# Kernel tuning notes

Hardware: AMD Instinct MI355X
Metric: run time of the kernel (lower is better)

## Reference

```python
import math
import jax, jax.numpy as jnp
import numpy as np

N_GRAPHS = 400
N_PER = 50
N = N_GRAPHS * N_PER          # 20000 nodes
K = 12                        # k_neighbors
E = N * K                     # 240000 edges
ND = 128                      # node_dim
TD = 128                      # time_dim
LD = 128                      # latent_dim
SD = 32                       # species_emb_dim
L = 4                         # num_layers


def _lin(key, fi, fo):
    return (jax.random.normal(key, (fi, fo), dtype=jnp.float32) / np.sqrt(fi)).astype(jnp.float32)


def setup_inputs() -> dict:
    rng = np.random.default_rng(0)
    coords = (rng.standard_normal((N_GRAPHS, N_PER, 3)) * 3.0).astype(np.float32)
    # exact kNN per graph (loop=False): dst = center node, src = neighbor
    d = ((coords[:, :, None, :] - coords[:, None, :, :]) ** 2).sum(-1)  # [G, n, n]
    ii = np.arange(N_PER)
    d[:, ii, ii] = np.inf
    nbr = np.argpartition(d, K, axis=-1)[:, :, :K]                      # [G, n, K]
    base = (np.arange(N_GRAPHS) * N_PER)[:, None, None]
    edge_src = (nbr + base).reshape(-1).astype(np.int64)
    edge_dst = (np.broadcast_to(ii[None, :, None], (N_GRAPHS, N_PER, K)) + base).reshape(-1).astype(np.int64)
    batch_indices = np.repeat(np.arange(N_GRAPHS), N_PER).astype(np.int64)

    key = jax.random.key(0)
    ks = jax.random.split(key, 32)
    inp = {
        'z_nodes': jax.random.normal(ks[0], (N, LD), dtype=jnp.float32),
        't': jax.random.uniform(ks[1], (N_GRAPHS,), dtype=jnp.float32) * 1000.0,
        'cart_coords': jnp.asarray(coords.reshape(N, 3)),
        'species': jax.random.randint(ks[2], (N,), 1, 119),
        'batch_indices': jnp.asarray(batch_indices),
        'edge_src': jnp.asarray(edge_src),
        'edge_dst': jnp.asarray(edge_dst),
        # parameters
        'species_emb': jax.random.normal(ks[3], (119, SD), dtype=jnp.float32),
        'tm_W1': _lin(ks[4], TD, 2 * TD), 'tm_b1': jnp.zeros((2 * TD,), jnp.float32),
        'tm_W2': _lin(ks[5], 2 * TD, TD), 'tm_b2': jnp.zeros((TD,), jnp.float32),
        'ne_W': _lin(ks[6], LD + SD, ND), 'ne_b': jnp.zeros((ND,), jnp.float32),
        'eW1': jnp.stack([_lin(jax.random.fold_in(ks[7], l), 2 * ND + 1 + TD, ND) for l in range(L)]),
        'eb1': jnp.zeros((L, ND), jnp.float32),
        'eW2': jnp.stack([_lin(jax.random.fold_in(ks[8], l), ND, ND) for l in range(L)]),
        'eb2': jnp.zeros((L, ND), jnp.float32),
        'cW1': jnp.stack([_lin(jax.random.fold_in(ks[9], l), ND, ND) for l in range(L)]),
        'cb1': jnp.zeros((L, ND), jnp.float32),
        'cW2': jnp.stack([_lin(jax.random.fold_in(ks[10], l), ND, 1) for l in range(L)]),
        'nW1': jnp.stack([_lin(jax.random.fold_in(ks[11], l), 2 * ND + TD, ND) for l in range(L)]),
        'nb1': jnp.zeros((L, ND), jnp.float32),
        'nW2': jnp.stack([_lin(jax.random.fold_in(ks[12], l), ND, ND) for l in range(L)]),
        'nb2': jnp.zeros((L, ND), jnp.float32),
    }
    return inp


def reference(z_nodes, t, cart_coords, species, batch_indices, edge_src, edge_dst,
              species_emb, tm_W1, tm_b1, tm_W2, tm_b2, ne_W, ne_b,
              eW1, eb1, eW2, eb2, cW1, cb1, cW2, nW1, nb1, nW2, nb2):
    silu = jax.nn.silu
    # sinusoidal time embedding + time MLP
    half = TD // 2
    freqs = jnp.exp(jnp.arange(half, dtype=jnp.float32) * (-math.log(10000.0) / (half - 1)))
    ang = t[:, None] * freqs[None, :]                     # [G, half]
    temb = jnp.concatenate([jnp.sin(ang), jnp.cos(ang)], axis=-1)
    temb = silu(temb @ tm_W1 + tm_b1) @ tm_W2 + tm_b2     # [G, TD]
    t_nodes = temb[batch_indices]                         # [N, TD]

    sp = species_emb[species]                             # [N, SD]
    h = jnp.concatenate([z_nodes, sp], axis=-1) @ ne_W + ne_b  # [N, ND]

    diff = cart_coords[edge_src] - cart_coords[edge_dst]  # [E, 3]
    dist_sq = jnp.sum(diff * diff, axis=-1, keepdims=True)  # [E, 1]
    dist = jnp.sqrt(dist_sq + 1e-8)
    t_edges = t_nodes[edge_src]                           # [E, TD]

    n = h.shape[0]
    total_shift = jnp.zeros_like(cart_coords)
    for l in range(L):
        edge_in = jnp.concatenate([h[edge_src], h[edge_dst], dist_sq, t_edges], axis=-1)
        m = silu(edge_in @ eW1[l] + eb1[l])
        m = silu(m @ eW2[l] + eb2[l])                     # [E, ND]
        gate = silu(m @ cW1[l] + cb1[l]) @ cW2[l]         # [E, 1]
        shift = diff / dist * gate                        # [E, 3]
        total_shift = total_shift + jax.ops.segment_sum(shift, edge_dst, num_segments=n)
        m_i = jax.ops.segment_sum(m, edge_dst, num_segments=n)  # [N, ND]
        node_in = jnp.concatenate([h, m_i, t_nodes], axis=-1)
        h = h + (silu(node_in @ nW1[l] + nb1[l]) @ nW2[l] + nb2[l])
    return (total_shift, h)
```

## Files before the change

kernel.cpp:

```cpp
#include <hip/hip_runtime.h>
#include <math.h>

#define GN 400
#define NPER 50
#define NN 20000
#define LL 4

typedef __attribute__((ext_vector_type(8))) short short8;
typedef __attribute__((ext_vector_type(4))) float f32x4;

__device__ __forceinline__ float fast_rcp(float x) {
#if __has_builtin(__builtin_amdgcn_rcpf)
  return __builtin_amdgcn_rcpf(x);
#else
  return 1.0f / x;
#endif
}
__device__ __forceinline__ float silu_f(float x) {
  return x * fast_rcp(1.0f + __expf(-x));
}
__device__ __forceinline__ unsigned short f2bu(float f) {
  unsigned int u = __float_as_uint(f);
  unsigned int r = (u + 0x7fffu + ((u >> 16) & 1u)) >> 16;
  return (unsigned short)r;
}
__device__ __forceinline__ unsigned int pack2bf(float lo, float hi) {
  unsigned int a = __float_as_uint(lo) + 0x8000u;
  unsigned int b = __float_as_uint(hi) + 0x8000u;
#if __has_builtin(__builtin_amdgcn_perm)
  return __builtin_amdgcn_perm(b, a, 0x07060302);
#else
  return (b & 0xffff0000u) | (a >> 16);
#endif
}
__device__ __forceinline__ float bhi(unsigned int u) { return __uint_as_float(u & 0xffff0000u); }
__device__ __forceinline__ float blo(unsigned int u) { return __uint_as_float(u << 16); }

__device__ __forceinline__ short8 pack8(const float* v) {
  union { unsigned int u[4]; short8 s; } t;
  t.u[0] = pack2bf(v[0], v[1]);
  t.u[1] = pack2bf(v[2], v[3]);
  t.u[2] = pack2bf(v[4], v[5]);
  t.u[3] = pack2bf(v[6], v[7]);
  return t.s;
}

__global__ __launch_bounds__(128) void time_kernel(
    const float* __restrict__ t,
    const float* __restrict__ tm_W1, const float* __restrict__ tm_b1,
    const float* __restrict__ tm_W2, const float* __restrict__ tm_b2,
    const float* __restrict__ eW1, const float* __restrict__ eb1,
    const float* __restrict__ nW1, const float* __restrict__ nb1,
    float* __restrict__ temb, float* __restrict__ tE, float* __restrict__ tN)
{
  int g = blockIdx.x;
  int j = threadIdx.x;
  __shared__ float x[128];
  __shared__ float hid[256];
  __shared__ float te[128];
  float tv = t[g];
  if (j < 64) {
    float f = __expf((float)j * (-9.210340371976184f / 63.0f));
    float a = tv * f;
    x[j] = sinf(a);
    x[j + 64] = cosf(a);
  }
  __syncthreads();
  for (int o = j; o < 256; o += 128) {
    float acc = tm_b1[o];
    for (int k = 0; k < 128; ++k) acc = fmaf(x[k], tm_W1[k * 256 + o], acc);
    hid[o] = silu_f(acc);
  }
  __syncthreads();
  {
    float acc = tm_b2[j];
    for (int k = 0; k < 256; ++k) acc = fmaf(hid[k], tm_W2[k * 128 + j], acc);
    te[j] = acc;
    temb[g * 128 + j] = acc;
  }
  __syncthreads();
  for (int l = 0; l < LL; ++l) {
    const float* W = eW1 + (l * 385 + 257) * 128;
    float acc = eb1[l * 128 + j];
    for (int k = 0; k < 128; ++k) acc = fmaf(te[k], W[k * 128 + j], acc);
    tE[(l * GN + g) * 128 + j] = acc;
    const float* Wn = nW1 + (l * 384 + 256) * 128;
    float acc2 = nb1[l * 128 + j];
    for (int k = 0; k < 128; ++k) acc2 = fmaf(te[k], Wn[k * 128 + j], acc2);
    tN[(l * GN + g) * 128 + j] = acc2;
  }
}

__global__ __launch_bounds__(256) void prep_transpose(
    const float* __restrict__ eW1, const float* __restrict__ eW2,
    const float* __restrict__ cW1, const float* __restrict__ nW1,
    const float* __restrict__ nW2, const float* __restrict__ ne_W,
    unsigned short* __restrict__ eABt, unsigned short* __restrict__ eW2t,
    unsigned short* __restrict__ cW1t, unsigned short* __restrict__ nW1t,
    unsigned short* __restrict__ nW2t, unsigned short* __restrict__ ne_Wt)
{
  __shared__ float tile[32][33];
  int j = blockIdx.y;
  const float* src;
  unsigned short* dst;
  int dstride = 128, Kj = 128;
  if (j < 28) {
    int l = j / 7, m = j % 7;
    switch (m) {
      case 0: src = eW1 + (l * 385 + 0) * 128;   dst = eABt + l * 256 * 128;             break;
      case 1: src = eW1 + (l * 385 + 128) * 128; dst = eABt + l * 256 * 128 + 128 * 128; break;
      case 2: src = eW2 + l * 16384;             dst = eW2t + l * 16384;                 break;
      case 3: src = cW1 + l * 16384;             dst = cW1t + l * 16384;                 break;
      case 4: src = nW1 + (l * 384 + 0) * 128;   dst = nW1t + l * 128 * 256; dstride = 256; break;
      case 5: src = nW1 + (l * 384 + 128) * 128; dst = nW1t + l * 128 * 256 + 128; dstride = 256; break;
      default: src = nW2 + l * 16384;            dst = nW2t + l * 16384;                 break;
    }
  } else {
    src = ne_W; dst = ne_Wt; dstride = 160; Kj = 160;
  }
  int gx = blockIdx.x;
  int tk = (gx % 5) * 32;
  int tn = (gx / 5) * 32;
  if (tk >= Kj) return;
  int ti = threadIdx.x >> 5, tj = threadIdx.x & 31;
#pragma unroll
  for (int p = 0; p < 4; ++p) {
    int i = ti + p * 8;
    tile[i][tj] = src[(tk + i) * 128 + tn + tj];
  }
  __syncthreads();
#pragma unroll
  for (int p = 0; p < 4; ++p) {
    int i = ti + p * 8;
    dst[(tn + i) * dstride + tk + tj] = f2bu(tile[tj][i]);
  }
}

__global__ __launch_bounds__(128) void edge_mfma(
    const unsigned short* __restrict__ hAB,
    const float* __restrict__ coords, const int* __restrict__ edge_src,
    const float* __restrict__ eW1,
    const unsigned short* __restrict__ eW2t, const float* __restrict__ eb2,
    const unsigned short* __restrict__ cW1t, const float* __restrict__ cb1,
    const float* __restrict__ cW2, const float* __restrict__ tE,
    unsigned short* __restrict__ m_i, float* __restrict__ shift_out,
    int l, int addflag)
{
  __shared__ unsigned short mbuf[2][48 * 136];
  __shared__ float sdir[2][48 * 4];
  __shared__ float sgate[2][48];

  int tid = threadIdx.x;
  int wv = tid >> 6;
  int l6 = tid & 63;
  int e16 = l6 & 15, q = l6 >> 4;
  int nbase = blockIdx.x * 8 + wv * 4;
  int ebase = nbase * 12;
  unsigned short* mb = mbuf[wv];
  float* sd = sdir[wv];
  float* sg = sgate[wv];

  const unsigned short* eW2t_l = eW2t + l * 16384;
  const unsigned short* cW1t_l = cW1t + l * 16384;
  const float* eb2_l = eb2 + l * 128;
  const float* cb1_l = cb1 + l * 128;
  const float* cW2_l = cW2 + l * 128;
  const float* tE_l = tE + l * GN * 128;
  const float* wd = eW1 + (l * 385 + 256) * 128;

  int ssrc[3], sdst[3];
  float sds[3];
#pragma unroll
  for (int grp = 0; grp < 3; ++grp) {
    int eloc = grp * 16 + e16;
    int e = ebase + eloc;
    int src = edge_src[e];
    src = min(max(src, 0), NN - 1);
    int dst = nbase + eloc / 12;
    float dx = coords[src * 3 + 0] - coords[dst * 3 + 0];
    float dy = coords[src * 3 + 1] - coords[dst * 3 + 1];
    float dz = coords[src * 3 + 2] - coords[dst * 3 + 2];
    float ds = dx * dx + dy * dy + dz * dz;
    float rinv = 1.0f / sqrtf(ds + 1e-8f);
    if (q == 0) {
      sd[eloc * 4 + 0] = dx * rinv;
      sd[eloc * 4 + 1] = dy * rinv;
      sd[eloc * 4 + 2] = dz * rinv;
    }
    ssrc[grp] = src; sdst[grp] = dst; sds[grp] = ds;
  }

  short8 bfr[3][4];
#pragma unroll
  for (int grp = 0; grp < 3; ++grp) {
    int g = sdst[grp] / NPER;
    float ds = sds[grp];
#pragma unroll
    for (int kc = 0; kc < 4; ++kc) {
      int k0 = kc * 32 + q * 8;
      uint4 ua = *(const uint4*)(hAB + ssrc[grp] * 256 + k0);
      uint4 ub = *(const uint4*)(hAB + sdst[grp] * 256 + 128 + k0);
      float4 w0 = *(const float4*)(wd + k0);
      float4 w1 = *(const float4*)(wd + k0 + 4);
      float4 t0 = *(const float4*)(tE_l + g * 128 + k0);
      float4 t1 = *(const float4*)(tE_l + g * 128 + k0 + 4);
      float v[8];
      v[0] = silu_f(blo(ua.x) + blo(ub.x) + ds * w0.x + t0.x);
      v[1] = silu_f(bhi(ua.x) + bhi(ub.x) + ds * w0.y + t0.y);
      v[2] = silu_f(blo(ua.y) + blo(ub.y) + ds * w0.z + t0.z);
      v[3] = silu_f(bhi(ua.y) + bhi(ub.y) + ds * w0.w + t0.w);
      v[4] = silu_f(blo(ua.z) + blo(ub.z) + ds * w1.x + t1.x);
      v[5] = silu_f(bhi(ua.z) + bhi(ub.z) + ds * w1.y + t1.y);
      v[6] = silu_f(blo(ua.w) + blo(ub.w) + ds * w1.z + t1.z);
      v[7] = silu_f(bhi(ua.w) + bhi(ub.w) + ds * w1.w + t1.w);
      bfr[grp][kc] = pack8(v);
    }
  }

#pragma unroll
  for (int mt = 0; mt < 8; ++mt) {
    short8 af[4];
#pragma unroll
    for (int kc = 0; kc < 4; ++kc)
      af[kc] = *(const short8*)(eW2t_l + (mt * 16 + e16) * 128 + kc * 32 + q * 8);
    f32x4 acc[3] = {(f32x4){0,0,0,0}, (f32x4){0,0,0,0}, (f32x4){0,0,0,0}};
#pragma unroll
    for (int kc = 0; kc < 4; ++kc) {
#pragma unroll
      for (int grp = 0; grp < 3; ++grp)
        acc[grp] = __builtin_amdgcn_mfma_f32_16x16x32_bf16(af[kc], bfr[grp][kc], acc[grp], 0, 0, 0);
    }
    float4 b4 = *(const float4*)(eb2_l + mt * 16 + q * 4);
#pragma unroll
    for (int grp = 0; grp < 3; ++grp) {
      float v0 = silu_f(acc[grp][0] + b4.x);
      float v1 = silu_f(acc[grp][1] + b4.y);
      float v2 = silu_f(acc[grp][2] + b4.z);
      float v3 = silu_f(acc[grp][3] + b4.w);
      uint2 p;
      p.x = pack2bf(v0, v1);
      p.y = pack2bf(v2, v3);
      *(uint2*)&mb[(grp * 16 + e16) * 136 + mt * 16 + q * 4] = p;
    }
  }
  __threadfence_block();

  short8 af2[3][4];
#pragma unroll
  for (int grp = 0; grp < 3; ++grp)
#pragma unroll
    for (int kc = 0; kc < 4; ++kc)
      af2[grp][kc] = *(const short8*)&mb[(grp * 16 + e16) * 136 + kc * 32 + q * 8];

  float gp[3][4] = {{0,0,0,0},{0,0,0,0},{0,0,0,0}};
#pragma unroll
  for (int ct = 0; ct < 8; ++ct) {
    short8 bf[4];
#pragma unroll
    for (int kc = 0; kc < 4; ++kc)
      bf[kc] = *(const short8*)(cW1t_l + (ct * 16 + e16) * 128 + kc * 32 + q * 8);
    f32x4 acc[3] = {(f32x4){0,0,0,0}, (f32x4){0,0,0,0}, (f32x4){0,0,0,0}};
#pragma unroll
    for (int kc = 0; kc < 4; ++kc) {
#pragma unroll
      for (int grp = 0; grp < 3; ++grp)
        acc[grp] = __builtin_amdgcn_mfma_f32_16x16x32_bf16(af2[grp][kc], bf[kc], acc[grp], 0, 0, 0);
    }
    float cb = cb1_l[ct * 16 + e16];
    float c2 = cW2_l[ct * 16 + e16];
#pragma unroll
    for (int grp = 0; grp < 3; ++grp)
#pragma unroll
      for (int r = 0; r < 4; ++r)
        gp[grp][r] += silu_f(acc[grp][r] + cb) * c2;
  }
#pragma unroll
  for (int grp = 0; grp < 3; ++grp)
#pragma unroll
    for (int r = 0; r < 4; ++r) {
      float v = gp[grp][r];
      v += __shfl_xor(v, 1);
      v += __shfl_xor(v, 2);
      v += __shfl_xor(v, 4);
      v += __shfl_xor(v, 8);
      if (e16 == 0) sg[grp * 16 + q * 4 + r] = v;
    }
  __threadfence_block();

  {
    int nl = q, c8 = e16 * 8;
    float s[8] = {0,0,0,0,0,0,0,0};
#pragma unroll
    for (int r = 0; r < 12; ++r) {
      uint4 u = *(const uint4*)&mb[(nl * 12 + r) * 136 + c8];
      s[0] += blo(u.x); s[1] += bhi(u.x);
      s[2] += blo(u.y); s[3] += bhi(u.y);
      s[4] += blo(u.z); s[5] += bhi(u.z);
      s[6] += blo(u.w); s[7] += bhi(u.w);
    }
    uint4 o;
    o.x = pack2bf(s[0], s[1]); o.y = pack2bf(s[2], s[3]);
    o.z = pack2bf(s[4], s[5]); o.w = pack2bf(s[6], s[7]);
    *(uint4*)(m_i + (nbase + nl) * 128 + c8) = o;
  }
  if (l6 < 12) {
    int nl = l6 / 3, c = l6 - nl * 3;
    float s = 0.f;
#pragma unroll
    for (int r = 0; r < 12; ++r) {
      int e = nl * 12 + r;
      s = fmaf(sd[e * 4 + c], sg[e], s);
    }
    int n = nbase + nl;
    if (addflag) shift_out[n * 3 + c] += s;
    else         shift_out[n * 3 + c] = s;
  }
}

__global__ __launch_bounds__(128) void node_mfma(
    float* __restrict__ h, const unsigned short* __restrict__ m_i,
    const unsigned short* __restrict__ nW1t_l, const unsigned short* __restrict__ nW2t_l,
    const float* __restrict__ nb2_l, const float* __restrict__ tN_l,
    const unsigned short* __restrict__ eABt_next, unsigned short* __restrict__ hAB,
    int has_c)
{
  __shared__ unsigned short z1buf[16 * 136];
  __shared__ unsigned short hbuf[16 * 136];
  int tid = threadIdx.x;
  int wv = tid >> 6, l6 = tid & 63;
  int e16 = l6 & 15, q = l6 >> 4;
  int row = blockIdx.x * 16 + e16;
  int g = row / NPER;

  short8 bfh[8];
#pragma unroll
  for (int kc = 0; kc < 8; ++kc) {
    int k0 = kc * 32 + q * 8;
    if (k0 < 128) {
      float4 f0 = *(const float4*)(h + row * 128 + k0);
      float4 f1 = *(const float4*)(h + row * 128 + k0 + 4);
      float v[8] = {f0.x, f0.y, f0.z, f0.w, f1.x, f1.y, f1.z, f1.w};
      bfh[kc] = pack8(v);
    } else {
      bfh[kc] = *(const short8*)(m_i + row * 128 + (k0 - 128));
    }
  }
#pragma unroll
  for (int mi = 0; mi < 4; ++mi) {
    int mt = wv * 4 + mi;
    short8 af[8];
#pragma unroll
    for (int kc = 0; kc < 8; ++kc)
      af[kc] = *(const short8*)(nW1t_l + (mt * 16 + e16) * 256 + kc * 32 + q * 8);
    f32x4 acc = (f32x4){0,0,0,0};
#pragma unroll
    for (int kc = 0; kc < 8; ++kc)
      acc = __builtin_amdgcn_mfma_f32_16x16x32_bf16(af[kc], bfh[kc], acc, 0, 0, 0);
    float4 tv = *(const float4*)(tN_l + g * 128 + mt * 16 + q * 4);
    float v0 = silu_f(acc[0] + tv.x);
    float v1 = silu_f(acc[1] + tv.y);
    float v2 = silu_f(acc[2] + tv.z);
    float v3 = silu_f(acc[3] + tv.w);
    uint2 p; p.x = pack2bf(v0, v1); p.y = pack2bf(v2, v3);
    *(uint2*)&z1buf[e16 * 136 + mt * 16 + q * 4] = p;
  }
  __syncthreads();

  short8 zf[4];
#pragma unroll
  for (int kc = 0; kc < 4; ++kc)
    zf[kc] = *(const short8*)&z1buf[e16 * 136 + kc * 32 + q * 8];
#pragma unroll
  for (int mi = 0; mi < 4; ++mi) {
    int mt = wv * 4 + mi;
    short8 af[4];
#pragma unroll
    for (int kc = 0; kc < 4; ++kc)
      af[kc] = *(const short8*)(nW2t_l + (mt * 16 + e16) * 128 + kc * 32 + q * 8);
    f32x4 acc = (f32x4){0,0,0,0};
#pragma unroll
    for (int kc = 0; kc < 4; ++kc)
      acc = __builtin_amdgcn_mfma_f32_16x16x32_bf16(af[kc], zf[kc], acc, 0, 0, 0);
    float4 hv = *(const float4*)(h + row * 128 + mt * 16 + q * 4);
    float4 b4 = *(const float4*)(nb2_l + mt * 16 + q * 4);
    float4 o;
    o.x = hv.x + acc[0] + b4.x;
    o.y = hv.y + acc[1] + b4.y;
    o.z = hv.z + acc[2] + b4.z;
    o.w = hv.w + acc[3] + b4.w;
    *(float4*)(h + row * 128 + mt * 16 + q * 4) = o;
    uint2 p; p.x = pack2bf(o.x, o.y); p.y = pack2bf(o.z, o.w);
    *(uint2*)&hbuf[e16 * 136 + mt * 16 + q * 4] = p;
  }
  if (has_c) {
    __syncthreads();
    short8 hf[4];
#pragma unroll
    for (int kc = 0; kc < 4; ++kc)
      hf[kc] = *(const short8*)&hbuf[e16 * 136 + kc * 32 + q * 8];
#pragma unroll
    for (int mi = 0; mi < 8; ++mi) {
      int mt = wv * 8 + mi;
      short8 af[4];
#pragma unroll
      for (int kc = 0; kc < 4; ++kc)
        af[kc] = *(const short8*)(eABt_next + (mt * 16 + e16) * 128 + kc * 32 + q * 8);
      f32x4 acc = (f32x4){0,0,0,0};
#pragma unroll
      for (int kc = 0; kc < 4; ++kc)
        acc = __builtin_amdgcn_mfma_f32_16x16x32_bf16(af[kc], hf[kc], acc, 0, 0, 0);
      uint2 p; p.x = pack2bf(acc[0], acc[1]); p.y = pack2bf(acc[2], acc[3]);
      *(uint2*)(hAB + row * 256 + mt * 16 + q * 4) = p;
    }
  }
}

__global__ __launch_bounds__(128) void encoder_mfma(
    const float* __restrict__ z, const int* __restrict__ species,
    const float* __restrict__ species_emb,
    const unsigned short* __restrict__ ne_Wt, const float* __restrict__ ne_b,
    const unsigned short* __restrict__ eABt0,
    float* __restrict__ h, unsigned short* __restrict__ hAB)
{
  __shared__ unsigned short hbuf[16 * 136];
  int tid = threadIdx.x;
  int wv = tid >> 6, l6 = tid & 63;
  int e16 = l6 & 15, q = l6 >> 4;
  int row = blockIdx.x * 16 + e16;
  int sp = species[row];
  sp = min(max(sp, 0), 118);

  short8 bfh[5];
#pragma unroll
  for (int kc = 0; kc < 5; ++kc) {
    int k0 = kc * 32 + q * 8;
    const float* src = (k0 < 128) ? (z + row * 128 + k0)
                                  : (species_emb + sp * 32 + (k0 - 128));
    float4 f0 = *(const float4*)src;
    float4 f1 = *(const float4*)(src + 4);
    float v[8] = {f0.x, f0.y, f0.z, f0.w, f1.x, f1.y, f1.z, f1.w};
    bfh[kc] = pack8(v);
  }
#pragma unroll
  for (int mi = 0; mi < 4; ++mi) {
    int mt = wv * 4 + mi;
    short8 af[5];
#pragma unroll
    for (int kc = 0; kc < 5; ++kc)
      af[kc] = *(const short8*)(ne_Wt + (mt * 16 + e16) * 160 + kc * 32 + q * 8);
    f32x4 acc = (f32x4){0,0,0,0};
#pragma unroll
    for (int kc = 0; kc < 5; ++kc)
      acc = __builtin_amdgcn_mfma_f32_16x16x32_bf16(af[kc], bfh[kc], acc, 0, 0, 0);
    float4 b4 = *(const float4*)(ne_b + mt * 16 + q * 4);
    float4 o;
    o.x = acc[0] + b4.x; o.y = acc[1] + b4.y;
    o.z = acc[2] + b4.z; o.w = acc[3] + b4.w;
    *(float4*)(h + row * 128 + mt * 16 + q * 4) = o;
    uint2 p; p.x = pack2bf(o.x, o.y); p.y = pack2bf(o.z, o.w);
    *(uint2*)&hbuf[e16 * 136 + mt * 16 + q * 4] = p;
  }
  __syncthreads();
  short8 hf[4];
#pragma unroll
  for (int kc = 0; kc < 4; ++kc)
    hf[kc] = *(const short8*)&hbuf[e16 * 136 + kc * 32 + q * 8];
#pragma unroll
  for (int mi = 0; mi < 8; ++mi) {
    int mt = wv * 8 + mi;
    short8 af[4];
#pragma unroll
    for (int kc = 0; kc < 4; ++kc)
      af[kc] = *(const short8*)(eABt0 + (mt * 16 + e16) * 128 + kc * 32 + q * 8);
    f32x4 acc = (f32x4){0,0,0,0};
#pragma unroll
    for (int kc = 0; kc < 4; ++kc)
      acc = __builtin_amdgcn_mfma_f32_16x16x32_bf16(af[kc], hf[kc], acc, 0, 0, 0);
    uint2 p; p.x = pack2bf(acc[0], acc[1]); p.y = pack2bf(acc[2], acc[3]);
    *(uint2*)(hAB + row * 256 + mt * 16 + q * 4) = p;
  }
}

extern "C" void kernel_launch(void* const* d_in, const int* in_sizes, int n_in,
                              void* d_out, int out_size, void* d_ws, size_t ws_size,
                              hipStream_t stream)
{
  const float* z_nodes     = (const float*)d_in[0];
  const float* t           = (const float*)d_in[1];
  const float* coords      = (const float*)d_in[2];
  const int*   species     = (const int*)d_in[3];
  const int*   edge_src    = (const int*)d_in[5];
  const float* species_emb = (const float*)d_in[7];
  const float* tm_W1 = (const float*)d_in[8];
  const float* tm_b1 = (const float*)d_in[9];
  const float* tm_W2 = (const float*)d_in[10];
  const float* tm_b2 = (const float*)d_in[11];
  const float* ne_W  = (const float*)d_in[12];
  const float* ne_b  = (const float*)d_in[13];
  const float* eW1   = (const float*)d_in[14];
  const float* eb1   = (const float*)d_in[15];
  const float* eW2   = (const float*)d_in[16];
  const float* eb2   = (const float*)d_in[17];
  const float* cW1   = (const float*)d_in[18];
  const float* cb1   = (const float*)d_in[19];
  const float* cW2   = (const float*)d_in[20];
  const float* nW1   = (const float*)d_in[21];
  const float* nb1   = (const float*)d_in[22];
  const float* nW2   = (const float*)d_in[23];
  const float* nb2   = (const float*)d_in[24];

  char* wsb = (char*)d_ws;
  float* temb = (float*)(wsb + 0);
  float* tEb  = (float*)(wsb + 204800);
  float* tNb  = (float*)(wsb + 1024000);
  unsigned short* hAB  = (unsigned short*)(wsb + 1843200);
  unsigned short* m_i  = (unsigned short*)(wsb + 12083200);
  unsigned short* eABt = (unsigned short*)(wsb + 17203200);
  unsigned short* eW2t = (unsigned short*)(wsb + 17465344);
  unsigned short* cW1t = (unsigned short*)(wsb + 17596416);
  unsigned short* nW1t = (unsigned short*)(wsb + 17727488);
  unsigned short* nW2t = (unsigned short*)(wsb + 17989632);
  unsigned short* ne_Wt= (unsigned short*)(wsb + 18120704);

  float* outp  = (float*)d_out;
  float* shift = outp;
  float* h     = outp + 60000;

  time_kernel<<<GN, 128, 0, stream>>>(t, tm_W1, tm_b1, tm_W2, tm_b2,
                                      eW1, eb1, nW1, nb1, temb, tEb, tNb);
  prep_transpose<<<dim3(20, 29), 256, 0, stream>>>(eW1, eW2, cW1, nW1, nW2, ne_W,
                                                   eABt, eW2t, cW1t, nW1t, nW2t, ne_Wt);
  encoder_mfma<<<NN / 16, 128, 0, stream>>>(z_nodes, species, species_emb,
                                            ne_Wt, ne_b, eABt, h, hAB);
  for (int l = 0; l < LL; ++l) {
    edge_mfma<<<NN / 8, 128, 0, stream>>>(hAB, coords, edge_src, eW1,
                                          eW2t, eb2, cW1t, cb1, cW2, tEb,
                                          m_i, shift, l, (l > 0) ? 1 : 0);
    int has_c = (l < LL - 1) ? 1 : 0;
    node_mfma<<<NN / 16, 128, 0, stream>>>(h, m_i,
                                           nW1t + l * 128 * 256, nW2t + l * 16384,
                                           nb2 + l * 128, tNb + l * GN * 128,
                                           has_c ? (eABt + (l + 1) * 256 * 128) : eABt,
                                           hAB, has_c);
  }
}
```

Baseline: 554.8 us.

## Give each wave its own 16-row tile in node/encoder kernels, drop block barriers

```diff
diff --git a/kernel.cpp b/kernel.cpp
--- a/kernel.cpp
+++ b/kernel.cpp
@@ -43,6 +43,13 @@
   t.u[2] = pack2bf(v[4], v[5]);
   t.u[3] = pack2bf(v[6], v[7]);
   return t.s;
+}
+__device__ __forceinline__ void wave_fence() {
+#if __has_builtin(__builtin_amdgcn_wave_barrier)
+  __builtin_amdgcn_wave_barrier();
+#else
+  __syncthreads();
+#endif
 }
 
 __global__ __launch_bounds__(128) void time_kernel(
@@ -243,7 +250,7 @@
       *(uint2*)&mb[(grp * 16 + e16) * 136 + mt * 16 + q * 4] = p;
     }
   }
-  __threadfence_block();
+  wave_fence();
 
   short8 af2[3][4];
 #pragma unroll
@@ -285,7 +292,7 @@
       v += __shfl_xor(v, 8);
       if (e16 == 0) sg[grp * 16 + q * 4 + r] = v;
     }
-  __threadfence_block();
+  wave_fence();
 
   {
     int nl = q, c8 = e16 * 8;
@@ -324,13 +331,15 @@
     const unsigned short* __restrict__ eABt_next, unsigned short* __restrict__ hAB,
     int has_c)
 {
-  __shared__ unsigned short z1buf[16 * 136];
-  __shared__ unsigned short hbuf[16 * 136];
+  __shared__ unsigned short z1buf[2][16 * 136];
+  __shared__ unsigned short hbuf[2][16 * 136];
   int tid = threadIdx.x;
   int wv = tid >> 6, l6 = tid & 63;
   int e16 = l6 & 15, q = l6 >> 4;
-  int row = blockIdx.x * 16 + e16;
+  int row = blockIdx.x * 32 + wv * 16 + e16;
   int g = row / NPER;
+  unsigned short* zb = z1buf[wv];
+  unsigned short* hb = hbuf[wv];
 
   short8 bfh[8];
 #pragma unroll
@@ -346,8 +355,7 @@
     }
   }
 #pragma unroll
-  for (int mi = 0; mi < 4; ++mi) {
-    int mt = wv * 4 + mi;
+  for (int mt = 0; mt < 8; ++mt) {
     short8 af[8];
 #pragma unroll
     for (int kc = 0; kc < 8; ++kc)
@@ -362,17 +370,16 @@
     float v2 = silu_f(acc[2] + tv.z);
     float v3 = silu_f(acc[3] + tv.w);
     uint2 p; p.x = pack2bf(v0, v1); p.y = pack2bf(v2, v3);
-    *(uint2*)&z1buf[e16 * 136 + mt * 16 + q * 4] = p;
-  }
-  __syncthreads();
+    *(uint2*)&zb[e16 * 136 + mt * 16 + q * 4] = p;
+  }
+  wave_fence();
 
   short8 zf[4];
 #pragma unroll
   for (int kc = 0; kc < 4; ++kc)
-    zf[kc] = *(const short8*)&z1buf[e16 * 136 + kc * 32 + q * 8];
-#pragma unroll
-  for (int mi = 0; mi < 4; ++mi) {
-    int mt = wv * 4 + mi;
+    zf[kc] = *(const short8*)&zb[e16 * 136 + kc * 32 + q * 8];
+#pragma unroll
+  for (int mt = 0; mt < 8; ++mt) {
     short8 af[4];
 #pragma unroll
     for (int kc = 0; kc < 4; ++kc)
@@ -390,17 +397,16 @@
     o.w = hv.w + acc[3] + b4.w;
     *(float4*)(h + row * 128 + mt * 16 + q * 4) = o;
     uint2 p; p.x = pack2bf(o.x, o.y); p.y = pack2bf(o.z, o.w);
-    *(uint2*)&hbuf[e16 * 136 + mt * 16 + q * 4] = p;
+    *(uint2*)&hb[e16 * 136 + mt * 16 + q * 4] = p;
   }
   if (has_c) {
-    __syncthreads();
+    wave_fence();
     short8 hf[4];
 #pragma unroll
     for (int kc = 0; kc < 4; ++kc)
-      hf[kc] = *(const short8*)&hbuf[e16 * 136 + kc * 32 + q * 8];
-#pragma unroll
-    for (int mi = 0; mi < 8; ++mi) {
-      int mt = wv * 8 + mi;
+      hf[kc] = *(const short8*)&hb[e16 * 136 + kc * 32 + q * 8];
+#pragma unroll
+    for (int mt = 0; mt < 16; ++mt) {
       short8 af[4];
 #pragma unroll
       for (int kc = 0; kc < 4; ++kc)
@@ -422,11 +428,12 @@
     const unsigned short* __restrict__ eABt0,
     float* __restrict__ h, unsigned short* __restrict__ hAB)
 {
-  __shared__ unsigned short hbuf[16 * 136];
+  __shared__ unsigned short hbuf[2][16 * 136];
   int tid = threadIdx.x;
   int wv = tid >> 6, l6 = tid & 63;
   int e16 = l6 & 15, q = l6 >> 4;
-  int row = blockIdx.x * 16 + e16;
+  int row = blockIdx.x * 32 + wv * 16 + e16;
+  unsigned short* hb = hbuf[wv];
   int sp = species[row];
   sp = min(max(sp, 0), 118);
 
@@ -442,8 +449,7 @@
     bfh[kc] = pack8(v);
   }
 #pragma unroll
-  for (int mi = 0; mi < 4; ++mi) {
-    int mt = wv * 4 + mi;
+  for (int mt = 0; mt < 8; ++mt) {
     short8 af[5];
 #pragma unroll
     for (int kc = 0; kc < 5; ++kc)
@@ -458,16 +464,15 @@
     o.z = acc[2] + b4.z; o.w = acc[3] + b4.w;
     *(float4*)(h + row * 128 + mt * 16 + q * 4) = o;
     uint2 p; p.x = pack2bf(o.x, o.y); p.y = pack2bf(o.z, o.w);
-    *(uint2*)&hbuf[e16 * 136 + mt * 16 + q * 4] = p;
-  }
-  __syncthreads();
+    *(uint2*)&hb[e16 * 136 + mt * 16 + q * 4] = p;
+  }
+  wave_fence();
   short8 hf[4];
 #pragma unroll
   for (int kc = 0; kc < 4; ++kc)
-    hf[kc] = *(const short8*)&hbuf[e16 * 136 + kc * 32 + q * 8];
-#pragma unroll
-  for (int mi = 0; mi < 8; ++mi) {
-    int mt = wv * 8 + mi;
+    hf[kc] = *(const short8*)&hb[e16 * 136 + kc * 32 + q * 8];
+#pragma unroll
+  for (int mt = 0; mt < 16; ++mt) {
     short8 af[4];
 #pragma unroll
     for (int kc = 0; kc < 4; ++kc)
@@ -530,14 +535,14 @@
                                       eW1, eb1, nW1, nb1, temb, tEb, tNb);
   prep_transpose<<<dim3(20, 29), 256, 0, stream>>>(eW1, eW2, cW1, nW1, nW2, ne_W,
                                                    eABt, eW2t, cW1t, nW1t, nW2t, ne_Wt);
-  encoder_mfma<<<NN / 16, 128, 0, stream>>>(z_nodes, species, species_emb,
+  encoder_mfma<<<NN / 32, 128, 0, stream>>>(z_nodes, species, species_emb,
                                             ne_Wt, ne_b, eABt, h, hAB);
   for (int l = 0; l < LL; ++l) {
     edge_mfma<<<NN / 8, 128, 0, stream>>>(hAB, coords, edge_src, eW1,
                                           eW2t, eb2, cW1t, cb1, cW2, tEb,
                                           m_i, shift, l, (l > 0) ? 1 : 0);
     int has_c = (l < LL - 1) ? 1 : 0;
-    node_mfma<<<NN / 16, 128, 0, stream>>>(h, m_i,
+    node_mfma<<<NN / 32, 128, 0, stream>>>(h, m_i,
                                            nW1t + l * 128 * 256, nW2t + l * 16384,
                                            nb2 + l * 128, tNb + l * GN * 128,
                                            has_c ? (eABt + (l + 1) * 256 * 128) : eABt,
```

Result: slower. 570.2 us (+2.8%).
